# Kernel optimization log

Measured on AMD Instinct MI355X. Metric: run time of the kernel, lower is better.

## Reference

```python
import jax, jax.numpy as jnp
import numpy as np

B, H, W = 64, 512, 512
T = 100           # num_thresholds
R = 8             # defect regions per image (max label id)
BLOCK = 128       # defect regions are 128x128 blocks on a 4x4 grid
SAT = 1.0         # saturation_threshold (relative)


def setup_inputs() -> dict:
    key = jax.random.key(0)
    k1, _ = jax.random.split(key)
    preds = jax.random.uniform(k1, (B, H, W), dtype=jnp.float32)
    thresholds = jnp.linspace(0.0, 1.0, T).astype(jnp.float32)
    # Build a labeled GT mask: R disjoint 128x128 block regions per image,
    # labels 1..R (0 = background). This plays the role of measure.label(target).
    rng = np.random.default_rng(0)
    labels = np.zeros((B, H, W), dtype=np.int32)
    gb = H // BLOCK           # 4 blocks per side -> 16 candidate blocks
    nblocks = gb * gb
    for b in range(B):
        chosen = rng.permutation(nblocks)[:R]
        for rid, blk in enumerate(chosen, start=1):
            r, c = divmod(int(blk), gb)
            labels[b, r * BLOCK:(r + 1) * BLOCK, c * BLOCK:(c + 1) * BLOCK] = rid
    return {"preds": preds, "thresholds": thresholds, "labels": jnp.asarray(labels)}


def reference(preds, thresholds, labels):
    # preds: (B,H,W) float32 in [0,1); thresholds: (T,) sorted; labels: (B,H,W) int32, 0=bg.
    Bn, Hn, Wn = preds.shape
    Tn = thresholds.shape[0]
    flat_s = preds.reshape(-1)
    flat_l = labels.reshape(-1)
    # bucket[p] = number of thresholds <= score[p]; pixel passes thr[t] iff bucket > t.
    bucket = jnp.searchsorted(thresholds, flat_s, side='right')  # int in [0, T]
    # ---- background FP / TN per threshold (exact counts via histogram) ----
    bg = (flat_l == 0).astype(jnp.int32)
    bg_hist = jax.ops.segment_sum(bg, bucket, num_segments=Tn + 1)  # (T+1,)
    bg_total = bg_hist.sum()
    fp = (bg_total - jnp.cumsum(bg_hist)[:Tn]).astype(jnp.float32)  # fp[t] = #bg with score>=thr[t]
    tn = bg_total.astype(jnp.float32) - fp
    # ---- per-region TP per threshold (segmented histogram) ----
    bidx = jnp.repeat(jnp.arange(Bn), Hn * Wn)
    seg = bidx * R + (flat_l - 1)              # region id in [0, B*R)
    comb = seg * (Tn + 1) + bucket
    NSEG = Bn * R * (Tn + 1)
    comb = jnp.where(flat_l > 0, comb, NSEG)   # dump bg pixels in overflow slot
    hist = jax.ops.segment_sum(jnp.ones_like(bucket, dtype=jnp.int32), comb,
                               num_segments=NSEG + 1)[:NSEG].reshape(Bn, R, Tn + 1)
    area = hist.sum(-1)                                       # (B,R) defect areas
    tp = (area[..., None] - jnp.cumsum(hist, -1)[..., :Tn]).astype(jnp.float32)  # (B,R,T)
    sat = jnp.maximum(area.astype(jnp.float32) * SAT, 1.0)    # relative saturation
    valid = (area > 0).astype(jnp.float32)                    # guard empty regions
    spro = jnp.minimum(tp / sat[..., None], 1.0) * valid[..., None]
    spro_sum = spro.sum((0, 1))                               # (T,)
    n_def = jnp.maximum(valid.sum(), 1.0)
    mean_spro = spro_sum / n_def
    # ---- AUC over FPR (max_fpr = 1.0) ----
    denom = fp + tn
    fpr = jnp.where(denom > 0, fp / jnp.maximum(denom, 1.0), 0.0)
    order = jnp.argsort(fpr)
    x = fpr[order]
    y = mean_spro[order]
    auc = jnp.sum((x[1:] - x[:-1]) * (y[1:] + y[:-1]) * 0.5)  # trapezoid rule
    return auc
```

## Files before the change

### kernel.cpp

```cpp
#include <hip/hip_runtime.h>

#define B_N 64
#define H_N 512
#define W_N 512
#define T_N 100
#define TB  101
#define R_N 8
#define NLAB 9
#define BLOCKS_PER_IMG 32
#define PIX_PER_IMG (H_N * W_N)
#define PIX_PER_BLOCK (PIX_PER_IMG / BLOCKS_PER_IMG)

__device__ __forceinline__ int bucket_of(float s) {
    const double C = 1.0 / 99.0;
    int k0 = (int)(s * 99.0f) + 1;
    float tlo = (float)((double)(k0 - 1) * C);
    float thi = (float)((double)k0 * C);
    return k0 - (s < tlo ? 1 : 0) + (s >= thi ? 1 : 0);
}

__global__ __launch_bounds__(256) void hist_kernel(
    const float* __restrict__ preds, const int* __restrict__ labels,
    int* __restrict__ region_hist,
    int* __restrict__ bg_hist)
{
    __shared__ int whist[4][NLAB * TB];

    const int tid  = threadIdx.x;
    const int wave = tid >> 6;

    for (int i = tid; i < 4 * NLAB * TB; i += 256) ((int*)whist)[i] = 0;
    __syncthreads();

    const int img   = blockIdx.x / BLOCKS_PER_IMG;
    const int chunk = blockIdx.x % BLOCKS_PER_IMG;
    const long base = (long)img * PIX_PER_IMG + (long)chunk * PIX_PER_BLOCK;
    const float4* p4 = (const float4*)(preds + base);
    const int4*   l4 = (const int4*)(labels + base);
    int* __restrict__ myh = whist[wave];

    const int iters = PIX_PER_BLOCK / (256 * 8);
    for (int it = 0; it < iters; ++it) {
        float4 pv0 = p4[(it * 2 + 0) * 256 + tid];
        float4 pv1 = p4[(it * 2 + 1) * 256 + tid];
        int4   lv0 = l4[(it * 2 + 0) * 256 + tid];
        int4   lv1 = l4[(it * 2 + 1) * 256 + tid];
        float ps[8] = {pv0.x, pv0.y, pv0.z, pv0.w, pv1.x, pv1.y, pv1.z, pv1.w};
        int   ls[8] = {lv0.x, lv0.y, lv0.z, lv0.w, lv1.x, lv1.y, lv1.z, lv1.w};
#pragma unroll
        for (int j = 0; j < 8; ++j) {
            int k = bucket_of(ps[j]);
            atomicAdd(&myh[ls[j] * TB + k], 1);
        }
    }
    __syncthreads();

    for (int i = tid; i < NLAB * TB; i += 256) {
        int v = whist[0][i] + whist[1][i] + whist[2][i] + whist[3][i];
        if (v) {
            int lab = i / TB;
            int t   = i - lab * TB;
            if (lab == 0)
                atomicAdd(&bg_hist[img * TB + t], v);
            else
                atomicAdd(&region_hist[(img * R_N + (lab - 1)) * TB + t], v);
        }
    }
}

__global__ __launch_bounds__(256) void region_kernel(
    const int* __restrict__ region_hist,
    float* __restrict__ spro_sum,
    int* __restrict__ n_def)
{
    __shared__ int   h_sh[R_N * TB];
    __shared__ float area_sh[R_N];
    const int img = blockIdx.x;
    const int tid = threadIdx.x;

    for (int i = tid; i < R_N * TB; i += 256)
        h_sh[i] = region_hist[img * (R_N * TB) + i];
    __syncthreads();

    if (tid < R_N) {
        int a = 0;
        for (int t = 0; t < TB; ++t) a += h_sh[tid * TB + t];
        area_sh[tid] = (float)a;
    }
    __syncthreads();

    if (tid < T_N) {
        float s = 0.0f;
#pragma unroll
        for (int r = 0; r < R_N; ++r) {
            int tp = 0;
            for (int k = tid + 1; k < TB; ++k) tp += h_sh[r * TB + k];
            float area  = area_sh[r];
            float sat   = fmaxf(area, 1.0f);
            float valid = (area > 0.0f) ? 1.0f : 0.0f;
            s += fminf((float)tp / sat, 1.0f) * valid;
        }
        atomicAdd(&spro_sum[tid], s);
    }
    if (tid == 0) {
        int v = 0;
        for (int r = 0; r < R_N; ++r) v += (area_sh[r] > 0.0f) ? 1 : 0;
        atomicAdd(n_def, v);
    }
}

__global__ __launch_bounds__(256) void final_kernel(
    const int* __restrict__ bg_hist,
    const float* __restrict__ spro_sum,
    const int* __restrict__ n_def,
    float* __restrict__ out)
{
    __shared__ int    stage[B_N * TB];
    __shared__ int    bgh[TB];
    __shared__ float  fpr_sh[T_N];
    __shared__ float  ms_sh[T_N];
    __shared__ int    order[T_N];
    __shared__ double contrib[T_N];
    const int tid = threadIdx.x;

    for (int i = tid; i < B_N * TB; i += 256) stage[i] = bg_hist[i];
    __syncthreads();

    if (tid < TB) {
        int s = 0;
        for (int b = 0; b < B_N; ++b) s += stage[b * TB + tid];
        bgh[tid] = s;
    }
    __syncthreads();

    if (tid < T_N) {
        int fp_i = 0;
        for (int k = tid + 1; k < TB; ++k) fp_i += bgh[k];
        int tot = fp_i;
        for (int k = 0; k <= tid; ++k) tot += bgh[k];
        float bgt = (float)tot;
        float fp  = (float)fp_i;
        fpr_sh[tid] = (bgt > 0.0f) ? fp / fmaxf(bgt, 1.0f) : 0.0f;
        float nd = fmaxf((float)(*n_def), 1.0f);
        ms_sh[tid] = spro_sum[tid] / nd;
    }
    __syncthreads();

    if (tid < T_N) {
        float v = fpr_sh[tid];
        int r = 0;
        for (int j = 0; j < T_N; ++j) {
            float u = fpr_sh[j];
            r += (u < v) | ((u == v) & (j < tid));
        }
        order[r] = tid;
    }
    __syncthreads();

    if (tid < T_N - 1) {
        int o0 = order[tid], o1 = order[tid + 1];
        double x0 = fpr_sh[o0], x1 = fpr_sh[o1];
        double y0 = ms_sh[o0],  y1 = ms_sh[o1];
        contrib[tid] = (x1 - x0) * (y0 + y1) * 0.5;
    } else if (tid < T_N) {
        contrib[tid] = 0.0;
    }
    __syncthreads();

    if (tid == 0) {
        double s = 0.0;
        for (int i = 0; i < T_N - 1; ++i) s += contrib[i];
        out[0] = (float)s;
    }
}

extern "C" void kernel_launch(void* const* d_in, const int* in_sizes, int n_in,
                              void* d_out, int out_size, void* d_ws, size_t ws_size,
                              hipStream_t stream) {
    const float* preds  = (const float*)d_in[0];
    const int*   labels = (const int*)d_in[2];
    float* out = (float*)d_out;

    int*   region_hist = (int*)d_ws;
    int*   bg_hist     = region_hist + B_N * R_N * TB;
    float* spro_sum    = (float*)(bg_hist + B_N * TB);
    int*   n_def       = (int*)(spro_sum + T_N);

    size_t zbytes = sizeof(int) * (size_t)(B_N * R_N * TB + B_N * TB)
                  + sizeof(float) * T_N + sizeof(int);
    hipMemsetAsync(d_ws, 0, zbytes, stream);

    hist_kernel<<<B_N * BLOCKS_PER_IMG, 256, 0, stream>>>(preds, labels,
                                                          region_hist, bg_hist);
    region_kernel<<<B_N, 256, 0, stream>>>(region_hist, spro_sum, n_def);
    final_kernel<<<1, 256, 0, stream>>>(bg_hist, spro_sum, n_def, out);
}
```

Baseline: 170.0 us.

## Prefetch next tile in histogram loop and fuse final reduction via last-block pattern

The histogram loop now software-pipelines its global loads, issuing the next iteration's float4/int4 loads before the current iteration's shared-memory atomics. The region and final kernels are merged into one post kernel, where the last block to finish (found with an agent-scope atomic counter) runs the AUC reduction. This removes one kernel launch and overlaps memory latency with atomic work. In exchange it raises register use and puts a global atomic counter on the critical path.

```diff
diff --git a/kernel.cpp b/kernel.cpp
--- a/kernel.cpp
+++ b/kernel.cpp
@@ -40,18 +40,22 @@
     int* __restrict__ myh = whist[wave];
 
     const int iters = PIX_PER_BLOCK / (256 * 8);
+
+    float4 pa = p4[tid], pb = p4[256 + tid];
+    int4   la = l4[tid], lb = l4[256 + tid];
     for (int it = 0; it < iters; ++it) {
-        float4 pv0 = p4[(it * 2 + 0) * 256 + tid];
-        float4 pv1 = p4[(it * 2 + 1) * 256 + tid];
-        int4   lv0 = l4[(it * 2 + 0) * 256 + tid];
-        int4   lv1 = l4[(it * 2 + 1) * 256 + tid];
-        float ps[8] = {pv0.x, pv0.y, pv0.z, pv0.w, pv1.x, pv1.y, pv1.z, pv1.w};
-        int   ls[8] = {lv0.x, lv0.y, lv0.z, lv0.w, lv1.x, lv1.y, lv1.z, lv1.w};
+        float4 na, nb; int4 nla, nlb;
+        if (it + 1 < iters) {
+            int o = (it * 2 + 2) * 256 + tid;
+            na  = p4[o]; nb  = p4[o + 256];
+            nla = l4[o]; nlb = l4[o + 256];
+        }
+        float ps[8] = {pa.x, pa.y, pa.z, pa.w, pb.x, pb.y, pb.z, pb.w};
+        int   ls[8] = {la.x, la.y, la.z, la.w, lb.x, lb.y, lb.z, lb.w};
 #pragma unroll
-        for (int j = 0; j < 8; ++j) {
-            int k = bucket_of(ps[j]);
-            atomicAdd(&myh[ls[j] * TB + k], 1);
-        }
+        for (int j = 0; j < 8; ++j)
+            atomicAdd(&myh[ls[j] * TB + bucket_of(ps[j])], 1);
+        pa = na; pb = nb; la = nla; lb = nlb;
     }
     __syncthreads();
 
@@ -68,13 +72,17 @@
     }
 }
 
-__global__ __launch_bounds__(256) void region_kernel(
+__global__ __launch_bounds__(256) void post_kernel(
     const int* __restrict__ region_hist,
+    const int* __restrict__ bg_hist,
     float* __restrict__ spro_sum,
-    int* __restrict__ n_def)
+    int* __restrict__ n_def,
+    int* __restrict__ done_ctr,
+    float* __restrict__ out)
 {
     __shared__ int   h_sh[R_N * TB];
     __shared__ float area_sh[R_N];
+    __shared__ int   last_sh;
     const int img = blockIdx.x;
     const int tid = threadIdx.x;
 
@@ -107,21 +115,22 @@
         for (int r = 0; r < R_N; ++r) v += (area_sh[r] > 0.0f) ? 1 : 0;
         atomicAdd(n_def, v);
     }
-}
-
-__global__ __launch_bounds__(256) void final_kernel(
-    const int* __restrict__ bg_hist,
-    const float* __restrict__ spro_sum,
-    const int* __restrict__ n_def,
-    float* __restrict__ out)
-{
+
+    __syncthreads();
+    if (tid == 0) {
+        int prev = __hip_atomic_fetch_add(done_ctr, 1, __ATOMIC_ACQ_REL,
+                                          __HIP_MEMORY_SCOPE_AGENT);
+        last_sh = (prev == B_N - 1) ? 1 : 0;
+    }
+    __syncthreads();
+    if (!last_sh) return;
+
     __shared__ int    stage[B_N * TB];
     __shared__ int    bgh[TB];
     __shared__ float  fpr_sh[T_N];
     __shared__ float  ms_sh[T_N];
     __shared__ int    order[T_N];
     __shared__ double contrib[T_N];
-    const int tid = threadIdx.x;
 
     for (int i = tid; i < B_N * TB; i += 256) stage[i] = bg_hist[i];
     __syncthreads();
@@ -141,8 +150,10 @@
         float bgt = (float)tot;
         float fp  = (float)fp_i;
         fpr_sh[tid] = (bgt > 0.0f) ? fp / fmaxf(bgt, 1.0f) : 0.0f;
-        float nd = fmaxf((float)(*n_def), 1.0f);
-        ms_sh[tid] = spro_sum[tid] / nd;
+        int   ndi = __hip_atomic_load(n_def, __ATOMIC_RELAXED, __HIP_MEMORY_SCOPE_AGENT);
+        float ss  = __hip_atomic_load(&spro_sum[tid], __ATOMIC_RELAXED, __HIP_MEMORY_SCOPE_AGENT);
+        float nd  = fmaxf((float)ndi, 1.0f);
+        ms_sh[tid] = ss / nd;
     }
     __syncthreads();
 
@@ -185,13 +196,14 @@
     int*   bg_hist     = region_hist + B_N * R_N * TB;
     float* spro_sum    = (float*)(bg_hist + B_N * TB);
     int*   n_def       = (int*)(spro_sum + T_N);
+    int*   done_ctr    = n_def + 1;
 
     size_t zbytes = sizeof(int) * (size_t)(B_N * R_N * TB + B_N * TB)
-                  + sizeof(float) * T_N + sizeof(int);
+                  + sizeof(float) * T_N + 2 * sizeof(int);
     hipMemsetAsync(d_ws, 0, zbytes, stream);
 
     hist_kernel<<<B_N * BLOCKS_PER_IMG, 256, 0, stream>>>(preds, labels,
                                                           region_hist, bg_hist);
-    region_kernel<<<B_N, 256, 0, stream>>>(region_hist, spro_sum, n_def);
-    final_kernel<<<1, 256, 0, stream>>>(bg_hist, spro_sum, n_def, out);
-}
+    post_kernel<<<B_N, 256, 0, stream>>>(region_hist, bg_hist, spro_sum,
+                                         n_def, done_ctr, out);
+}
```

Result: no change. 168.1 us (-1.1%).
